# Kernel optimization log

Hardware: AMD Instinct MI355X
Metric: run time of the kernel (lower is better)

The kernel has to match this reference:

```python
import jax, jax.numpy as jnp
import numpy as np

B, T, DIM = 1, 2048, 1024
NUM_HEADS, HEAD_DIM = 8, 128
ATTN_SCALE = 0.12


def _rms_norm(x):
    # F.rms_norm(x, x.size(-1)) with no weight; eps defaults to machine eps
    eps = jnp.asarray(jnp.finfo(x.dtype).eps, x.dtype)
    return x * jax.lax.rsqrt(jnp.mean(x * x, axis=-1, keepdims=True) + eps)


def _rotary_tables(seq_len, head_dim):
    # (1/1024) ** linspace(0,1,head_dim//4), then pad with head_dim//4 zeros
    freq = (1.0 / 1024.0) ** jnp.linspace(0.0, 1.0, head_dim // 4, dtype=jnp.float32)
    ang = jnp.concatenate([freq, jnp.zeros(head_dim // 4, jnp.float32)])  # [hd/2]
    theta = jnp.arange(seq_len, dtype=jnp.float32)[:, None] * ang[None, :]  # [T, hd/2]
    return jnp.cos(theta), jnp.sin(theta)


def _apply_rotary(x, cos, sin):
    # x: [B, T, H, hd]
    x1, x2 = jnp.split(x.astype(jnp.float32), 2, axis=-1)
    c = cos[None, :, None, :]
    s = sin[None, :, None, :]
    y1 = x1 * c + x2 * s
    y2 = -x1 * s + x2 * c
    return jnp.concatenate([y1, y2], axis=-1).astype(x.dtype)


def setup_inputs() -> dict:
    key = jax.random.key(0)
    ks = jax.random.split(key, 5)
    bound = (3.0 ** 0.5) * 0.5 * DIM ** (-0.5)
    x = jax.random.normal(ks[0], (B, T, DIM), jnp.float32)
    ve = jax.random.normal(ks[1], (B, T, NUM_HEADS * HEAD_DIM), jnp.float32)
    qkv_w = jax.random.uniform(ks[2], (3, NUM_HEADS * HEAD_DIM, DIM), jnp.float32, -bound, bound)
    lambdas = jnp.array([0.5, 0.5], jnp.float32)
    # original zero-inits c_proj; use small random weight so the output is nontrivial
    c_proj_w = jax.random.uniform(ks[3], (DIM, NUM_HEADS * HEAD_DIM), jnp.float32, -bound, bound)
    return {"x": x, "ve": ve, "qkv_w": qkv_w, "lambdas": lambdas, "c_proj_w": c_proj_w}


def reference(x, ve, qkv_w, lambdas, c_proj_w):
    Bx, Tx, D = x.shape
    H, hd = NUM_HEADS, HEAD_DIM
    # fused QKV projection: weight [3*H*hd, D]
    qkv = x @ qkv_w.reshape(3 * H * hd, D).T            # [B, T, 3*H*hd]
    qkv = qkv.reshape(Bx, Tx, 3 * H, hd)
    q, k, v = jnp.split(qkv, 3, axis=-2)                # each [B, T, H, hd]
    q, k = _rms_norm(q), _rms_norm(k)
    cos, sin = _rotary_tables(Tx, hd)
    q, k = _apply_rotary(q, cos, sin), _apply_rotary(k, cos, sin)
    v = lambdas[0] * v + lambdas[1] * ve.reshape(v.shape)
    att = jnp.einsum('bthd,bshd->bhts', q, k) * ATTN_SCALE
    causal = jnp.tril(jnp.ones((Tx, Tx), bool))
    att = jnp.where(causal[None, None], att, -jnp.inf)
    att = jax.nn.softmax(att, axis=-1)
    y = jnp.einsum('bhts,bshd->bthd', att, v).reshape(Bx, Tx, H * hd)
    return y @ c_proj_w.T
```

## Files before the change

kernel.cpp:

```cpp
#include <hip/hip_runtime.h>


typedef __attribute__((ext_vector_type(8))) short short8;
typedef __attribute__((ext_vector_type(4))) short short4b;
typedef __attribute__((ext_vector_type(4))) float fx4;
typedef __attribute__((ext_vector_type(8))) unsigned short ushort8;
typedef __attribute__((ext_vector_type(4))) unsigned short ushort4v;
typedef __attribute__((ext_vector_type(2))) unsigned short ushort2v;
typedef __attribute__((ext_vector_type(4))) float float4v;

#define T_SEQ 2048
#define NH 8
#define HD 128

__device__ __forceinline__ unsigned short f2bf(float f) {
  union { float f; unsigned u; } v; v.f = f;
  unsigned u = v.u;
  u += 0x7fffu + ((u >> 16) & 1u);
  return (unsigned short)(u >> 16);
}
__device__ __forceinline__ short bf_t(float f) {
  union { float f; unsigned u; } v; v.f = f;
  return (short)(v.u >> 16);
}
__device__ __forceinline__ float bf2f(unsigned short h) {
  union { unsigned u; float f; } v; v.u = ((unsigned)h) << 16;
  return v.f;
}

typedef __attribute__((address_space(1))) unsigned int glb_u32;
typedef __attribute__((address_space(3))) unsigned int lds_u32;
__device__ __forceinline__ void gl_lds16(const unsigned short* g, unsigned short* l) {
  __builtin_amdgcn_global_load_lds((const glb_u32*)g, (lds_u32*)l, 16, 0, 0);
}

__global__ __launch_bounds__(256) void cast3_kernel(
    const float* __restrict__ x, const float* __restrict__ w1,
    const float* __restrict__ w2, unsigned short* __restrict__ o) {
  long q = (long)blockIdx.x * 256 + threadIdx.x;
  const float* src;
  if (q < 524288)        src = x  + 4 * q;
  else if (q < 1310720)  src = w1 + 4 * (q - 524288);
  else                   src = w2 + 4 * (q - 1310720);
  float4v v = *(const float4v*)src;
  ushort4v r;
  r[0] = f2bf(v[0]); r[1] = f2bf(v[1]); r[2] = f2bf(v[2]); r[3] = f2bf(v[3]);
  *(ushort4v*)(o + 4 * q) = r;
}

template <bool OUT_BF16, int BM, int BN>
__global__ __launch_bounds__(256) void gemm_bt4(
    const unsigned short* __restrict__ A, const unsigned short* __restrict__ B,
    void* __restrict__ Cp, int M, int N, int K) {
  constexpr int MT = BM / 32;
  constexpr int NT = BN / 32;
  constexpr int ASEG = BM / 8;
  constexpr int NLOAD = (BM + BN) / 32;
  __shared__ unsigned short a_sh[2][BM * 64];
  __shared__ unsigned short b_sh[2][BN * 64];
  const int tid = threadIdx.x;
  const int wave = tid >> 6, lane = tid & 63;
  const int ln = lane & 15, quad = lane >> 4;
  const int wm = wave & 1, wn = wave >> 1;
  const long arow0 = (long)blockIdx.y * BM;
  const long brow0 = (long)blockIdx.x * BN;

  const unsigned short* gsrc[NLOAD];
  unsigned short* ldst[NLOAD];
  int bstr[NLOAD];
  for (int i = 0; i < NLOAD; ++i) {
    int s = wave * NLOAD + i;
    int isB = s >= ASEG;
    int srel = isB ? s - ASEG : s;
    int li = srel * 64 + lane;
    int row = li >> 3, posc = li & 7;
    int c = posc ^ (row & 7);
    gsrc[i] = (isB ? B + brow0 * (long)K : A + arow0 * (long)K)
              + (long)row * K + c * 8;
    ldst[i] = (isB ? &b_sh[0][0] : &a_sh[0][0]) + srel * 512;
    bstr[i] = isB ? BN * 64 : BM * 64;
  }
  for (int i = 0; i < NLOAD; ++i) gl_lds16(gsrc[i], ldst[i]);

  fx4 acc[MT][NT] = {};
  int cur = 0;
  for (int k0 = 0; k0 < K; k0 += 64, cur ^= 1) {
    __syncthreads();
    if (k0 + 64 < K)
      for (int i = 0; i < NLOAD; ++i)
        gl_lds16(gsrc[i] + k0 + 64, ldst[i] + (cur ^ 1) * bstr[i]);
    const unsigned short* ash = &a_sh[cur][0];
    const unsigned short* bsh = &b_sh[cur][0];
    short8 af[2][MT], bfr[2][NT];
    for (int kq = 0; kq < 2; ++kq) {
      for (int mt = 0; mt < MT; ++mt) {
        int m = wm * (BM / 2) + mt * 16 + ln;
        int pos = (kq * 4 + quad) ^ (m & 7);
        af[kq][mt] = *(const short8*)&ash[m * 64 + pos * 8];
      }
      for (int nt = 0; nt < NT; ++nt) {
        int n = wn * (BN / 2) + nt * 16 + ln;
        int pos = (kq * 4 + quad) ^ (n & 7);
        bfr[kq][nt] = *(const short8*)&bsh[n * 64 + pos * 8];
      }
    }
    for (int kq = 0; kq < 2; ++kq)
      for (int mt = 0; mt < MT; ++mt)
        for (int nt = 0; nt < NT; ++nt)
          acc[mt][nt] = __builtin_amdgcn_mfma_f32_16x16x32_bf16(
              af[kq][mt], bfr[kq][nt], acc[mt][nt], 0, 0, 0);
  }
  for (int mt = 0; mt < MT; ++mt)
    for (int nt = 0; nt < NT; ++nt)
      for (int r = 0; r < 4; ++r) {
        long row = arow0 + wm * (BM / 2) + mt * 16 + quad * 4 + r;
        long col = brow0 + wn * (BN / 2) + nt * 16 + ln;
        float v = acc[mt][nt][r];
        if constexpr (OUT_BF16)
          ((unsigned short*)Cp)[row * N + col] = f2bf(v);
        else
          ((float*)Cp)[row * N + col] = v;
      }
}

__global__ __launch_bounds__(256) void prep_qkv(
    const unsigned short* __restrict__ qkv, const float* __restrict__ ve,
    const float* __restrict__ lambdas, unsigned short* __restrict__ qh,
    unsigned short* __restrict__ kh, unsigned short* __restrict__ vt) {
  __shared__ unsigned short lt[128 * 72];
  const int tt = blockIdx.x, h = blockIdx.y;
  const int tid = threadIdx.x;

  {
    const int r2 = tid >> 5, c = tid & 31;
    float ang[2];
    for (int u = 0; u < 2; ++u) {
      int dd = 2 * c + u;
      ang[u] = (dd < 32) ? exp2f(-10.0f * (float)dd / 31.0f) : 0.0f;
    }
    for (int rr = 0; rr < 8; ++rr) {
      int t = tt * 64 + rr * 8 + r2;
      float cv[2], sv[2];
      for (int u = 0; u < 2; ++u) {
        float th = (float)t * ang[u];
        sv[u] = __sinf(th); cv[u] = __cosf(th);
      }
      for (int which = 0; which < 2; ++which) {
        const unsigned short* src = qkv + (long)t * 3072 + which * 1024 + h * 128;
        ushort2v aa = *(const ushort2v*)(src + 2 * c);
        ushort2v bb = *(const ushort2v*)(src + 64 + 2 * c);
        float x1[2] = { bf2f(aa[0]), bf2f(aa[1]) };
        float x2[2] = { bf2f(bb[0]), bf2f(bb[1]) };
        float ss = x1[0]*x1[0] + x1[1]*x1[1] + x2[0]*x2[0] + x2[1]*x2[1];
        for (int off = 1; off < 32; off <<= 1) ss += __shfl_xor(ss, off);
        float rn = rsqrtf(ss * (1.0f / 128.0f) + 1.1920929e-7f);
        ushort2v o1, o2;
        for (int u = 0; u < 2; ++u) {
          float y1 = ( x1[u] * cv[u] + x2[u] * sv[u]) * rn;
          float y2 = (-x1[u] * sv[u] + x2[u] * cv[u]) * rn;
          o1[u] = f2bf(y1); o2[u] = f2bf(y2);
        }
        unsigned short* dst = (which ? kh : qh) + ((long)h * T_SEQ + t) * 128;
        *(ushort2v*)(dst + 2 * c) = o1;
        *(ushort2v*)(dst + 64 + 2 * c) = o2;
      }
    }
  }

  {
    const float l0 = lambdas[0], l1 = lambdas[1];
    const int r = tid >> 2, cb = (tid & 3) * 32;
    const unsigned short* vs = qkv + (long)(tt * 64 + r) * 3072 + 2048 + h * 128 + cb;
    const float* es = ve + (long)(tt * 64 + r) * 1024 + h * 128 + cb;
    ushort8 vv[4];
    for (int q = 0; q < 4; ++q) vv[q] = *(const ushort8*)(vs + 8 * q);
    float4v ee[8];
    for (int q = 0; q < 8; ++q) ee[q] = *(const float4v*)(es + 4 * q);
    for (int j = 0; j < 32; ++j) {
      float v = bf2f(vv[j >> 3][j & 7]) * l0 + ee[j >> 2][j & 3] * l1;
      lt[(cb + j) * 72 + r] = f2bf(v);
    }
    __syncthreads();
    const int d = tid >> 1, half = tid & 1;
    unsigned short* dst = vt + ((long)h * HD + d) * T_SEQ + tt * 64 + half * 32;
    const unsigned short* srcl = &lt[d * 72];
    for (int g = 0; g < 8; ++g) {
      int p0 = half * 32 + g * 4;
      int kv0 = ((p0 >> 5) & 1) * 32 + ((p0 >> 2) & 1) * 16 + ((p0 >> 3) & 3) * 4;
      *(ushort4v*)(dst + g * 4) = *(const ushort4v*)(srcl + kv0);
    }
  }
}

#define ATT_C1 0.17312340490667562f
#define ATT_C2 23.083120654223415f

__global__ __launch_bounds__(256, 2) void attn_part(
    const unsigned short* __restrict__ qh, const unsigned short* __restrict__ kh,
    const unsigned short* __restrict__ vt, unsigned short* __restrict__ Yp,
    float* __restrict__ lp) {
  __shared__ unsigned short kbuf[2][8192];
  __shared__ unsigned short vbuf[2][8192];
  const int tid = threadIdx.x;
  const int wave = tid >> 6, lane = tid & 63;
  const int ln = lane & 15, quad = lane >> 4;
  const int qt = blockIdx.x, h = blockIdx.y, ch = blockIdx.z;
  const int jmax = 2 * qt + 1;
  const int j0 = ch * 4;
  if (j0 > jmax) return;
  const int j1 = min(j0 + 3, jmax);

  int qg[2];
  short8 qf[2][4];
  for (int s = 0; s < 2; ++s) {
    qg[s] = qt * 128 + wave * 32 + s * 16 + ln;
    const unsigned short* qbase = qh + ((long)h * T_SEQ + qg[s]) * 128;
    for (int kc = 0; kc < 4; ++kc)
      qf[s][kc] = *(const short8*)(qbase + kc * 32 + quad * 8);
  }
  fx4 accy[2][8] = {};
  float l_loc[2] = {0.f, 0.f};

  const unsigned short* kg[4]; unsigned short* kl[4];
  const unsigned short* vg[4]; unsigned short* vl[4];
  for (int i = 0; i < 4; ++i) {
    int s = wave * 4 + i;
    { int li = s * 64 + lane; int row = li >> 4, posc = li & 15;
      int c = posc ^ (row & 15);
      kg[i] = kh + ((long)h * T_SEQ + row) * 128 + c * 8;
      kl[i] = &kbuf[0][s * 512]; }
    { int li = s * 64 + lane; int row = li >> 3, posc = li & 7;
      int c = posc ^ (row & 7);
      vg[i] = vt + ((long)h * HD + row) * T_SEQ + c * 8;
      vl[i] = &vbuf[0][s * 512]; }
  }
  for (int i = 0; i < 4; ++i) gl_lds16(kg[i] + (long)j0 * 8192, kl[i]);
  for (int i = 0; i < 4; ++i) gl_lds16(vg[i] + (long)j0 * 64, vl[i]);

  int cur = 0;
  for (int jt = j0; jt <= j1; ++jt, cur ^= 1) {
    __syncthreads();
    if (jt < j1) {
      int nb = (cur ^ 1) * 8192;
      for (int i = 0; i < 4; ++i) gl_lds16(kg[i] + (long)(jt + 1) * 8192, kl[i] + nb);
      for (int i = 0; i < 4; ++i) gl_lds16(vg[i] + (long)(jt + 1) * 64, vl[i] + nb);
    }
    const unsigned short* kb_ = &kbuf[cur][0];
    fx4 s4[2][4];
    for (int kt = 0; kt < 4; ++kt) {
      s4[0][kt] = fx4{0.f, 0.f, 0.f, 0.f};
      s4[1][kt] = fx4{0.f, 0.f, 0.f, 0.f};
      for (int kc = 0; kc < 4; ++kc) {
        int pos = (kc * 4 + quad) ^ ln;
        short8 kf = *(const short8*)&kb_[(kt * 16 + ln) * 128 + pos * 8];
        s4[0][kt] = __builtin_amdgcn_mfma_f32_16x16x32_bf16(kf, qf[0][kc], s4[0][kt], 0, 0, 0);
        s4[1][kt] = __builtin_amdgcn_mfma_f32_16x16x32_bf16(kf, qf[1][kc], s4[1][kt], 0, 0, 0);
      }
    }
    short4b pb[2][4];
    for (int s = 0; s < 2; ++s)
      for (int kt = 0; kt < 4; ++kt) {
        int kvb = jt * 64 + kt * 16 + quad * 4;
        float p[4];
        for (int r = 0; r < 4; ++r)
          p[r] = exp2f(fmaf(s4[s][kt][r], ATT_C1, -ATT_C2));
        if (jt * 64 + kt * 16 + 15 > qt * 128 + wave * 32 + s * 16) {
          for (int r = 0; r < 4; ++r) if (kvb + r > qg[s]) p[r] = 0.f;
        }
        l_loc[s] += (p[0] + p[1]) + (p[2] + p[3]);
        pb[s][kt] = short4b{ bf_t(p[0]), bf_t(p[1]), bf_t(p[2]), bf_t(p[3]) };
      }
    const unsigned short* vb_ = &vbuf[cur][0];
    for (int kh2 = 0; kh2 < 2; ++kh2) {
      for (int dt = 0; dt < 8; ++dt) {
        int row = dt * 16 + ln;
        int pos = (kh2 * 4 + quad) ^ (ln & 7);
        short8 va = *(const short8*)&vb_[row * 64 + pos * 8];
        short4b va0 = { va[0], va[1], va[2], va[3] };
        short4b va1 = { va[4], va[5], va[6], va[7] };
        for (int s = 0; s < 2; ++s) {
          accy[s][dt] = __builtin_amdgcn_mfma_f32_16x16x16bf16_1k(
              va0, pb[s][kh2 * 2], accy[s][dt], 0, 0, 0);
          accy[s][dt] = __builtin_amdgcn_mfma_f32_16x16x16bf16_1k(
              va1, pb[s][kh2 * 2 + 1], accy[s][dt], 0, 0, 0);
        }
      }
    }
  }

  int cbase = qt + ((qt - 1) * (qt - 1)) / 4;
  const long pp = (long)(h * 72 + cbase + ch);
  for (int s = 0; s < 2; ++s) {
    float l = l_loc[s];
    l += __shfl_xor(l, 16);
    l += __shfl_xor(l, 32);
    int q = wave * 32 + s * 16 + ln;
    if (quad == 0) lp[pp * 128 + q] = l;
    unsigned short* yb = Yp + pp * 16384 + (long)q * 128;
    for (int dt = 0; dt < 8; ++dt) {
      ushort4v o;
      for (int r = 0; r < 4; ++r) o[r] = f2bf(accy[s][dt][r]);
      *(ushort4v*)(yb + dt * 16 + quad * 4) = o;
    }
  }
}

__global__ __launch_bounds__(256) void attn_combine(
    const unsigned short* __restrict__ Yp, const float* __restrict__ lp,
    unsigned short* __restrict__ y) {
  const int bx = blockIdx.x, h = blockIdx.y;
  const int qt = bx >> 1, sub = bx & 1;
  const int tid = threadIdx.x;
  const int row = sub * 64 + (tid >> 2), cb = (tid & 3) * 32;
  const int nc = (qt >> 1) + 1;
  const int cbase = qt + ((qt - 1) * (qt - 1)) / 4;
  float acc[32];
  for (int j = 0; j < 32; ++j) acc[j] = 0.f;
  float ltot = 0.f;
  for (int c = 0; c < nc; ++c) {
    long pp = (long)(h * 72 + cbase + c);
    const unsigned short* ys = Yp + pp * 16384 + (long)row * 128 + cb;
    ltot += lp[pp * 128 + row];
    for (int q8 = 0; q8 < 4; ++q8) {
      ushort8 v = *(const ushort8*)(ys + q8 * 8);
      for (int j = 0; j < 8; ++j) acc[q8 * 8 + j] += bf2f(v[j]);
    }
  }
  float inv = 1.f / ltot;
  unsigned short* dst = y + (long)(qt * 128 + row) * 1024 + h * 128 + cb;
  for (int q8 = 0; q8 < 4; ++q8) {
    ushort8 o;
    for (int j = 0; j < 8; ++j) o[j] = f2bf(acc[q8 * 8 + j] * inv);
    *(ushort8*)(dst + q8 * 8) = o;
  }
}

extern "C" void kernel_launch(void* const* d_in, const int* in_sizes, int n_in,
                              void* d_out, int out_size, void* d_ws, size_t ws_size,
                              hipStream_t stream) {
  const float* x       = (const float*)d_in[0];
  const float* ve      = (const float*)d_in[1];
  const float* qkv_w   = (const float*)d_in[2];
  const float* lambdas = (const float*)d_in[3];
  const float* c_proj  = (const float*)d_in[4];
  char* ws = (char*)d_ws;
  unsigned short* qkv_bf = (unsigned short*)(ws);
  unsigned short* x_bf   = (unsigned short*)(ws + 12582912);
  unsigned short* wqkv   = (unsigned short*)(ws + 16777216);
  unsigned short* wproj  = (unsigned short*)(ws + 23068672);
  unsigned short* qhat   = (unsigned short*)(ws + 25165824);
  unsigned short* khat   = (unsigned short*)(ws + 29360128);
  unsigned short* vtb    = (unsigned short*)(ws + 33554432);
  unsigned short* ybf    = (unsigned short*)(ws + 37748736);
  unsigned short* Yp     = (unsigned short*)(ws);
  float*          lpart  = (float*)(ws + 18874368);
  float* out = (float*)d_out;

  cast3_kernel<<<6144, 256, 0, stream>>>(x, qkv_w, c_proj, x_bf);
  gemm_bt4<true, 64, 128><<<dim3(24, 32), 256, 0, stream>>>(x_bf, wqkv, qkv_bf, 2048, 3072, 1024);
  prep_qkv<<<dim3(32, 8), 256, 0, stream>>>(qkv_bf, ve, lambdas, qhat, khat, vtb);
  attn_part<<<dim3(16, 8, 8), 256, 0, stream>>>(qhat, khat, vtb, Yp, lpart);
  attn_combine<<<dim3(32, 8), 256, 0, stream>>>(Yp, lpart, ybf);
  gemm_bt4<false, 64, 64><<<dim3(16, 32), 256, 0, stream>>>(ybf, wproj, out, 2048, 1024, 1024);
}
```

Before: 194.6 us.

## Parameterize GEMM K-tile, retile QKV GEMM, split prep into two kernels

The GEMM template gains a BK parameter with a matching LDS swizzle. The QKV projection now uses 128x128 tiles with BK=32, which gives fewer, larger blocks. The fused prep kernel is split into a one-wave-per-(token, head, q/k) norm+rope kernel with far more parallelism and a separate V combine/transpose kernel. The aim is better GEMM reuse and better occupancy for the prep stage, at the cost of one extra launch and a changed swizzle that may add LDS bank conflicts. The output projection keeps BK=64 but now uses the new swizzle pattern.

```diff
diff --git a/kernel.cpp b/kernel.cpp
--- a/kernel.cpp
+++ b/kernel.cpp
@@ -48,16 +48,18 @@
   *(ushort4v*)(o + 4 * q) = r;
 }
 
-template <bool OUT_BF16, int BM, int BN>
-__global__ __launch_bounds__(256) void gemm_bt4(
+template <bool OUT_BF16, int BM, int BN, int BK>
+__global__ __launch_bounds__(256) void gemm_bt5(
     const unsigned short* __restrict__ A, const unsigned short* __restrict__ B,
     void* __restrict__ Cp, int M, int N, int K) {
   constexpr int MT = BM / 32;
   constexpr int NT = BN / 32;
-  constexpr int ASEG = BM / 8;
-  constexpr int NLOAD = (BM + BN) / 32;
-  __shared__ unsigned short a_sh[2][BM * 64];
-  __shared__ unsigned short b_sh[2][BN * 64];
+  constexpr int KQ = BK / 32;
+  constexpr int CPR = BK / 8;
+  constexpr int ASEG = BM * BK / 512;
+  constexpr int NLOAD = (BM + BN) * BK / 512 / 4;
+  __shared__ unsigned short a_sh[2][BM * BK];
+  __shared__ unsigned short b_sh[2][BN * BK];
   const int tid = threadIdx.x;
   const int wave = tid >> 6, lane = tid & 63;
   const int ln = lane & 15, quad = lane >> 4;
@@ -73,38 +75,38 @@
     int isB = s >= ASEG;
     int srel = isB ? s - ASEG : s;
     int li = srel * 64 + lane;
-    int row = li >> 3, posc = li & 7;
-    int c = posc ^ (row & 7);
+    int row = li / CPR, posc = li % CPR;
+    int c = posc ^ ((row >> 1) & (CPR - 1));
     gsrc[i] = (isB ? B + brow0 * (long)K : A + arow0 * (long)K)
               + (long)row * K + c * 8;
     ldst[i] = (isB ? &b_sh[0][0] : &a_sh[0][0]) + srel * 512;
-    bstr[i] = isB ? BN * 64 : BM * 64;
+    bstr[i] = (isB ? BN : BM) * BK;
   }
   for (int i = 0; i < NLOAD; ++i) gl_lds16(gsrc[i], ldst[i]);
 
   fx4 acc[MT][NT] = {};
   int cur = 0;
-  for (int k0 = 0; k0 < K; k0 += 64, cur ^= 1) {
+  for (int k0 = 0; k0 < K; k0 += BK, cur ^= 1) {
     __syncthreads();
-    if (k0 + 64 < K)
+    if (k0 + BK < K)
       for (int i = 0; i < NLOAD; ++i)
-        gl_lds16(gsrc[i] + k0 + 64, ldst[i] + (cur ^ 1) * bstr[i]);
+        gl_lds16(gsrc[i] + k0 + BK, ldst[i] + (cur ^ 1) * bstr[i]);
     const unsigned short* ash = &a_sh[cur][0];
     const unsigned short* bsh = &b_sh[cur][0];
-    short8 af[2][MT], bfr[2][NT];
-    for (int kq = 0; kq < 2; ++kq) {
+    short8 af[KQ][MT], bfr[KQ][NT];
+    for (int kq = 0; kq < KQ; ++kq) {
       for (int mt = 0; mt < MT; ++mt) {
         int m = wm * (BM / 2) + mt * 16 + ln;
-        int pos = (kq * 4 + quad) ^ (m & 7);
-        af[kq][mt] = *(const short8*)&ash[m * 64 + pos * 8];
+        int pos = (kq * 4 + quad) ^ ((m >> 1) & (CPR - 1));
+        af[kq][mt] = *(const short8*)&ash[m * BK + pos * 8];
       }
       for (int nt = 0; nt < NT; ++nt) {
         int n = wn * (BN / 2) + nt * 16 + ln;
-        int pos = (kq * 4 + quad) ^ (n & 7);
-        bfr[kq][nt] = *(const short8*)&bsh[n * 64 + pos * 8];
-      }
-    }
-    for (int kq = 0; kq < 2; ++kq)
+        int pos = (kq * 4 + quad) ^ ((n >> 1) & (CPR - 1));
+        bfr[kq][nt] = *(const short8*)&bsh[n * BK + pos * 8];
+      }
+    }
+    for (int kq = 0; kq < KQ; ++kq)
       for (int mt = 0; mt < MT; ++mt)
         for (int nt = 0; nt < NT; ++nt)
           acc[mt][nt] = __builtin_amdgcn_mfma_f32_16x16x32_bf16(
@@ -123,72 +125,54 @@
       }
 }
 
-__global__ __launch_bounds__(256) void prep_qkv(
+__global__ __launch_bounds__(256) void qk_norm_rope2(
+    const unsigned short* __restrict__ qkv, unsigned short* __restrict__ qh,
+    unsigned short* __restrict__ kh) {
+  const int idx = blockIdx.x * 4 + (threadIdx.x >> 6);
+  const int lane = threadIdx.x & 63;
+  const int which = idx & 1, h = (idx >> 1) & 7, t = idx >> 4;
+  const unsigned short* src = qkv + (long)t * 3072 + which * 1024 + h * 128;
+  float x1 = bf2f(src[lane]);
+  float x2 = bf2f(src[64 + lane]);
+  float ss = x1 * x1 + x2 * x2;
+  for (int off = 1; off < 64; off <<= 1) ss += __shfl_xor(ss, off);
+  float rn = rsqrtf(ss * (1.0f / 128.0f) + 1.1920929e-7f);
+  float ang = (lane < 32) ? exp2f(-10.0f * (float)lane / 31.0f) : 0.0f;
+  float th = (float)t * ang;
+  float sv = __sinf(th), cv = __cosf(th);
+  float y1 = ( x1 * cv + x2 * sv) * rn;
+  float y2 = (-x1 * sv + x2 * cv) * rn;
+  unsigned short* dst = (which ? kh : qh) + ((long)h * T_SEQ + t) * 128;
+  dst[lane] = f2bf(y1);
+  dst[64 + lane] = f2bf(y2);
+}
+
+__global__ __launch_bounds__(256) void v_combine_t(
     const unsigned short* __restrict__ qkv, const float* __restrict__ ve,
-    const float* __restrict__ lambdas, unsigned short* __restrict__ qh,
-    unsigned short* __restrict__ kh, unsigned short* __restrict__ vt) {
+    const float* __restrict__ lambdas, unsigned short* __restrict__ vt) {
   __shared__ unsigned short lt[128 * 72];
   const int tt = blockIdx.x, h = blockIdx.y;
   const int tid = threadIdx.x;
-
-  {
-    const int r2 = tid >> 5, c = tid & 31;
-    float ang[2];
-    for (int u = 0; u < 2; ++u) {
-      int dd = 2 * c + u;
-      ang[u] = (dd < 32) ? exp2f(-10.0f * (float)dd / 31.0f) : 0.0f;
-    }
-    for (int rr = 0; rr < 8; ++rr) {
-      int t = tt * 64 + rr * 8 + r2;
-      float cv[2], sv[2];
-      for (int u = 0; u < 2; ++u) {
-        float th = (float)t * ang[u];
-        sv[u] = __sinf(th); cv[u] = __cosf(th);
-      }
-      for (int which = 0; which < 2; ++which) {
-        const unsigned short* src = qkv + (long)t * 3072 + which * 1024 + h * 128;
-        ushort2v aa = *(const ushort2v*)(src + 2 * c);
-        ushort2v bb = *(const ushort2v*)(src + 64 + 2 * c);
-        float x1[2] = { bf2f(aa[0]), bf2f(aa[1]) };
-        float x2[2] = { bf2f(bb[0]), bf2f(bb[1]) };
-        float ss = x1[0]*x1[0] + x1[1]*x1[1] + x2[0]*x2[0] + x2[1]*x2[1];
-        for (int off = 1; off < 32; off <<= 1) ss += __shfl_xor(ss, off);
-        float rn = rsqrtf(ss * (1.0f / 128.0f) + 1.1920929e-7f);
-        ushort2v o1, o2;
-        for (int u = 0; u < 2; ++u) {
-          float y1 = ( x1[u] * cv[u] + x2[u] * sv[u]) * rn;
-          float y2 = (-x1[u] * sv[u] + x2[u] * cv[u]) * rn;
-          o1[u] = f2bf(y1); o2[u] = f2bf(y2);
-        }
-        unsigned short* dst = (which ? kh : qh) + ((long)h * T_SEQ + t) * 128;
-        *(ushort2v*)(dst + 2 * c) = o1;
-        *(ushort2v*)(dst + 64 + 2 * c) = o2;
-      }
-    }
-  }
-
-  {
-    const float l0 = lambdas[0], l1 = lambdas[1];
-    const int r = tid >> 2, cb = (tid & 3) * 32;
-    const unsigned short* vs = qkv + (long)(tt * 64 + r) * 3072 + 2048 + h * 128 + cb;
-    const float* es = ve + (long)(tt * 64 + r) * 1024 + h * 128 + cb;
-    ushort8 vv[4];
-    for (int q = 0; q < 4; ++q) vv[q] = *(const ushort8*)(vs + 8 * q);
-    float4v ee[8];
-    for (int q = 0; q < 8; ++q) ee[q] = *(const float4v*)(es + 4 * q);
-    for (int j = 0; j < 32; ++j) {
-      float v = bf2f(vv[j >> 3][j & 7]) * l0 + ee[j >> 2][j & 3] * l1;
-      lt[(cb + j) * 72 + r] = f2bf(v);
-    }
-    __syncthreads();
-    const int d = tid >> 1, half = tid & 1;
-    unsigned short* dst = vt + ((long)h * HD + d) * T_SEQ + tt * 64 + half * 32;
-    const unsigned short* srcl = &lt[d * 72];
-    for (int g = 0; g < 8; ++g) {
-      int p0 = half * 32 + g * 4;
-      int kv0 = ((p0 >> 5) & 1) * 32 + ((p0 >> 2) & 1) * 16 + ((p0 >> 3) & 3) * 4;
-      *(ushort4v*)(dst + g * 4) = *(const ushort4v*)(srcl + kv0);
-    }
+  const float l0 = lambdas[0], l1 = lambdas[1];
+  const int r = tid >> 2, cb = (tid & 3) * 32;
+  const unsigned short* vs = qkv + (long)(tt * 64 + r) * 3072 + 2048 + h * 128 + cb;
+  const float* es = ve + (long)(tt * 64 + r) * 1024 + h * 128 + cb;
+  ushort8 vv[4];
+  for (int q = 0; q < 4; ++q) vv[q] = *(const ushort8*)(vs + 8 * q);
+  float4v ee[8];
+  for (int q = 0; q < 8; ++q) ee[q] = *(const float4v*)(es + 4 * q);
+  for (int j = 0; j < 32; ++j) {
+    float v = bf2f(vv[j >> 3][j & 7]) * l0 + ee[j >> 2][j & 3] * l1;
+    lt[(cb + j) * 72 + r] = f2bf(v);
+  }
+  __syncthreads();
+  const int d = tid >> 1, half = tid & 1;
+  unsigned short* dst = vt + ((long)h * HD + d) * T_SEQ + tt * 64 + half * 32;
+  const unsigned short* srcl = &lt[d * 72];
+  for (int g = 0; g < 8; ++g) {
+    int p0 = half * 32 + g * 4;
+    int kv0 = ((p0 >> 5) & 1) * 32 + ((p0 >> 2) & 1) * 16 + ((p0 >> 3) & 3) * 4;
+    *(ushort4v*)(dst + g * 4) = *(const ushort4v*)(srcl + kv0);
   }
 }
 
@@ -357,9 +341,10 @@
   float* out = (float*)d_out;
 
   cast3_kernel<<<6144, 256, 0, stream>>>(x, qkv_w, c_proj, x_bf);
-  gemm_bt4<true, 64, 128><<<dim3(24, 32), 256, 0, stream>>>(x_bf, wqkv, qkv_bf, 2048, 3072, 1024);
-  prep_qkv<<<dim3(32, 8), 256, 0, stream>>>(qkv_bf, ve, lambdas, qhat, khat, vtb);
+  gemm_bt5<true, 128, 128, 32><<<dim3(24, 16), 256, 0, stream>>>(x_bf, wqkv, qkv_bf, 2048, 3072, 1024);
+  qk_norm_rope2<<<8192, 256, 0, stream>>>(qkv_bf, qhat, khat);
+  v_combine_t<<<dim3(32, 8), 256, 0, stream>>>(qkv_bf, ve, lambdas, vtb);
   attn_part<<<dim3(16, 8, 8), 256, 0, stream>>>(qhat, khat, vtb, Yp, lpart);
   attn_combine<<<dim3(32, 8), 256, 0, stream>>>(Yp, lpart, ybf);
-  gemm_bt4<false, 64, 64><<<dim3(16, 32), 256, 0, stream>>>(ybf, wproj, out, 2048, 1024, 1024);
-}
+  gemm_bt5<false, 64, 64, 64><<<dim3(16, 32), 256, 0, stream>>>(ybf, wproj, out, 2048, 1024, 1024);
+}
```

Measured after the change: 198.3 us. Within noise of the previous version (+1.9%).
